# Performance work log

Measured on AMD Instinct MI355X. Metric: run time of the kernel, lower is better.

Reference implementation:

```python
import jax, jax.numpy as jnp
import numpy as np

N_HEAD = 16
D_HEAD = 64
D_MODEL = 1024
QLEN = 1024
BSZ = 4
RLEN = 1024
CONV = 7
SCALE = 1.0 / D_HEAD ** 0.5
NEG = -1e30
EPS = 1e-5


def setup_inputs() -> dict:
    key = jax.random.key(0)
    ks = jax.random.split(key, 14)
    s = 0.02
    inp = {
        "w": jax.random.normal(ks[0], (QLEN, BSZ, D_MODEL), jnp.float32),
        "r": jax.random.normal(ks[1], (RLEN, D_MODEL), jnp.float32),
        "r_w_bias": jax.random.normal(ks[2], (N_HEAD, D_HEAD), jnp.float32) * s,
        "r_r_bias": jax.random.normal(ks[3], (N_HEAD, D_HEAD), jnp.float32) * s,
        "W_qkv": jax.random.normal(ks[4], (3 * N_HEAD * D_HEAD, D_MODEL), jnp.float32) * s,
        "W_r": jax.random.normal(ks[5], (N_HEAD * D_HEAD, D_MODEL), jnp.float32) * s,
        "W_o": jax.random.normal(ks[6], (D_MODEL, N_HEAD * D_HEAD), jnp.float32) * s,
        "conv_wq": jax.random.normal(ks[7], (D_HEAD, D_HEAD, CONV), jnp.float32) * s,
        "conv_bq": jax.random.normal(ks[8], (D_HEAD,), jnp.float32) * s,
        "conv_wk": jax.random.normal(ks[9], (D_HEAD, D_HEAD, CONV), jnp.float32) * s,
        "conv_bk": jax.random.normal(ks[10], (D_HEAD,), jnp.float32) * s,
        "conv_wv": jax.random.normal(ks[11], (D_HEAD, D_HEAD, CONV), jnp.float32) * s,
        "conv_bv": jax.random.normal(ks[12], (D_HEAD,), jnp.float32) * s,
        "ln_gamma": jnp.ones((D_MODEL,), jnp.float32),
        "ln_beta": jnp.zeros((D_MODEL,), jnp.float32),
        # causal mask, True = masked out (original dim==3 branch: [qlen, klen, 1])
        "attn_mask": jnp.triu(jnp.ones((QLEN, QLEN), bool), k=1)[:, :, None],
    }
    return inp


def _conv1d(x, wgt, b):
    # x: [N, C, L], wgt: [O, I, K] (torch Conv1d layout), same padding
    y = jax.lax.conv_general_dilated(x, wgt, (1,), [(CONV // 2, CONV // 2)],
                                     dimension_numbers=("NCH", "OIH", "NCH"))
    return y + b[None, :, None]


def _rel_shift(x):
    # x: [q, k, b, n] -> Transformer-XL relative shift
    q, k, b, n = x.shape
    xp = jnp.concatenate([jnp.zeros((q, 1, b, n), x.dtype), x], axis=1)
    return xp.reshape(k + 1, q, b, n)[1:].reshape(q, k, b, n)


def reference(w, r, r_w_bias, r_r_bias, W_qkv, W_r, W_o,
              conv_wq, conv_bq, conv_wk, conv_bk, conv_wv, conv_bv,
              ln_gamma, ln_beta, attn_mask):
    qlen, bsz, _ = w.shape
    klen = qlen  # mems=None

    heads = jnp.einsum('qbm,hm->qbh', w, W_qkv)  # [q, b, 3*n*d]
    hq, hk, hv = jnp.split(heads, 3, axis=-1)

    def to_conv(x, L):
        # [L, b, n*d] -> [n*b, d, L]
        return x.reshape(L, bsz, N_HEAD, D_HEAD).transpose(2, 1, 3, 0).reshape(N_HEAD * bsz, D_HEAD, L)

    def from_conv(x, L):
        # [n*b, d, L] -> [L, b, n, d]
        return x.reshape(N_HEAD, bsz, D_HEAD, L).transpose(3, 1, 0, 2)

    q_h = from_conv(_conv1d(to_conv(hq, qlen), conv_wq, conv_bq), qlen)
    k_h = from_conv(_conv1d(to_conv(hk, klen), conv_wk, conv_bk), klen)
    v_h = from_conv(_conv1d(to_conv(hv, klen), conv_wv, conv_bv), klen)

    r_head_k = (r @ W_r.T).reshape(-1, N_HEAD, D_HEAD)  # [rlen, n, d]

    AC = jnp.einsum('ibnd,jbnd->ijbn', q_h + r_w_bias, k_h)
    BD = _rel_shift(jnp.einsum('ibnd,jnd->ijbn', q_h + r_r_bias, r_head_k))
    score = (AC + BD) * SCALE
    score = jnp.where(attn_mask[:, :, :, None], NEG, score)

    prob = jax.nn.softmax(score, axis=1)
    vec = jnp.einsum('ijbn,jbnd->ibnd', prob, v_h).reshape(qlen, bsz, N_HEAD * D_HEAD)
    attn_out = vec @ W_o.T

    x = w + attn_out
    mu = jnp.mean(x, axis=-1, keepdims=True)
    var = jnp.mean(jnp.square(x - mu), axis=-1, keepdims=True)
    return (x - mu) / jnp.sqrt(var + EPS) * ln_gamma + ln_beta
```

## Files before the change

### kernel.cpp

```cpp
#include <hip/hip_runtime.h>
#include <math.h>

#define L 1024
#define SCALEF 0.125f
#define NEGF -1e30f

typedef unsigned short u16;
typedef __bf16 bf16x8 __attribute__((ext_vector_type(8)));
typedef float f32x4 __attribute__((ext_vector_type(4)));
typedef unsigned short u16x8 __attribute__((ext_vector_type(8)));
typedef unsigned short u16x4 __attribute__((ext_vector_type(4)));

#define MFMA(a, b, c) __builtin_amdgcn_mfma_f32_16x16x32_bf16(a, b, c, 0, 0, 0)

__device__ inline u16 f2b(float f) {
  union { float f; unsigned u; } v; v.f = f;
  unsigned r = v.u + 0x7fffu + ((v.u >> 16) & 1u);
  return (u16)(r >> 16);
}

__device__ __forceinline__ void ld16(u16* lds, const u16* g) {
  __builtin_amdgcn_global_load_lds((const __attribute__((address_space(1))) unsigned int*)g,
                                   (__attribute__((address_space(3))) unsigned int*)lds, 16, 0, 0);
}

__global__ __launch_bounds__(256) void prep(const float* __restrict__ w, const float* __restrict__ Wqkv,
                                            const float* __restrict__ r, const float* __restrict__ Wr,
                                            const float* __restrict__ Wo,
                                            const float* __restrict__ cwq, const float* __restrict__ cwk,
                                            const float* __restrict__ cwv,
                                            u16* w_bf, u16* wqkv_bf, u16* r_bf, u16* wr_bf, u16* wo_bf,
                                            u16* wTq, u16* wTk, u16* wTv) {
  int i = blockIdx.x * 256 + threadIdx.x;
  if (i < 2621440) {
    const float* s; u16* d; int off;
    if (i < 1048576)      { s = w;    d = w_bf;    off = i; }
    else if (i < 1835008) { s = Wqkv; d = wqkv_bf; off = i - 1048576; }
    else if (i < 2097152) { s = r;    d = r_bf;    off = i - 1835008; }
    else if (i < 2359296) { s = Wr;   d = wr_bf;   off = i - 2097152; }
    else                  { s = Wo;   d = wo_bf;   off = i - 2359296; }
    float4 v = ((const float4*)s)[off];
    u16x4 o = {f2b(v.x), f2b(v.y), f2b(v.z), f2b(v.w)};
    ((u16x4*)d)[off] = o;
  } else {
    int j = i - 2621440;
    if (j < 86016) {
      int z = j / 28672, rem = j % 28672;
      const float* src = z == 0 ? cwq : z == 1 ? cwk : cwv;
      u16* dst = z == 0 ? wTq : z == 1 ? wTk : wTv;
      int tt = rem >> 12, rem2 = rem & 4095;
      int dout = rem2 >> 6, din = rem2 & 63;
      dst[rem] = f2b(src[(dout * 64 + din) * 7 + tt]);
    }
  }
}

template <int OB>
__device__ __forceinline__ void gemm256_tile(u16* lds, const u16* __restrict__ A,
                                             const u16* __restrict__ B, void* Cp,
                                             int N, int m0, int n0) {
  int t = threadIdx.x;
  int wv = t >> 6, lane = t & 63;
  int q4 = lane >> 4, li = lane & 15;
  int wm = wv >> 2, wn = wv & 3;
  int pc = (q4 ^ ((li >> 1) & 3)) << 3;
  int cs = (((t & 3) ^ ((t >> 3) & 3)) << 3);
  const u16* Ab = A + (size_t)(m0 + (t >> 2)) * 1024 + cs;
  const u16* Bb = B + (size_t)(n0 + (t >> 2)) * 1024 + cs;
  int wo = wv * 512;
  f32x4 acc[8][4];
#pragma unroll
  for (int m = 0; m < 8; ++m)
#pragma unroll
    for (int n = 0; n < 4; ++n) acc[m][n] = (f32x4){0.f, 0.f, 0.f, 0.f};
#define STAGE_A(kt) { int sl = ((kt) & 3) * 16384, kb = (kt) * 32; \
    ld16(lds + sl + wo, Ab + kb); ld16(lds + sl + 4096 + wo, Ab + 131072 + kb); }
#define STAGE_B(kt) { int sl = ((kt) & 3) * 16384 + 8192, kb = (kt) * 32; \
    ld16(lds + sl + wo, Bb + kb); ld16(lds + sl + 4096 + wo, Bb + 131072 + kb); }
  STAGE_A(0); STAGE_B(0); STAGE_A(1); STAGE_B(1);
  asm volatile("s_waitcnt vmcnt(4)" ::: "memory");
  __builtin_amdgcn_s_barrier();
  for (int kt = 0; kt < 32; ++kt) {
    const u16* sA = lds + (kt & 3) * 16384;
    const u16* sB = sA + 8192;
    bf16x8 fa[4], fb[4];
#pragma unroll
    for (int m = 0; m < 4; ++m) fa[m] = *(const bf16x8*)&sA[(wm * 128 + m * 16 + li) * 32 + pc];
#pragma unroll
    for (int n = 0; n < 4; ++n) fb[n] = *(const bf16x8*)&sB[(wn * 64 + n * 16 + li) * 32 + pc];
    if (kt < 30) STAGE_A(kt + 2);
    __builtin_amdgcn_s_barrier();
    __builtin_amdgcn_s_setprio(1);
#pragma unroll
    for (int m = 0; m < 4; ++m)
#pragma unroll
      for (int n = 0; n < 4; ++n) acc[m][n] = MFMA(fa[m], fb[n], acc[m][n]);
    __builtin_amdgcn_s_setprio(0);
    __builtin_amdgcn_s_barrier();
    bf16x8 fa2[4];
#pragma unroll
    for (int m = 0; m < 4; ++m) fa2[m] = *(const bf16x8*)&sA[(wm * 128 + 64 + m * 16 + li) * 32 + pc];
    if (kt < 30) {
      STAGE_B(kt + 2);
      asm volatile("s_waitcnt vmcnt(4)" ::: "memory");
    } else {
      asm volatile("s_waitcnt vmcnt(0)" ::: "memory");
    }
    __builtin_amdgcn_s_barrier();
    __builtin_amdgcn_s_setprio(1);
#pragma unroll
    for (int m = 0; m < 4; ++m)
#pragma unroll
      for (int n = 0; n < 4; ++n) acc[4 + m][n] = MFMA(fa2[m], fb[n], acc[4 + m][n]);
    __builtin_amdgcn_s_setprio(0);
    __builtin_amdgcn_s_barrier();
  }
#undef STAGE_A
#undef STAGE_B
#pragma unroll
  for (int m = 0; m < 8; ++m)
#pragma unroll
    for (int r = 0; r < 4; ++r) {
      size_t row = m0 + wm * 128 + m * 16 + q4 * 4 + r;
      if (OB) {
        u16* C = (u16*)Cp;
#pragma unroll
        for (int n = 0; n < 4; ++n) C[row * N + n0 + wn * 64 + n * 16 + li] = f2b(acc[m][n][r]);
      } else {
        float* C = (float*)Cp;
#pragma unroll
        for (int n = 0; n < 4; ++n) C[row * N + n0 + wn * 64 + n * 16 + li] = acc[m][n][r];
      }
    }
}

__global__ __launch_bounds__(512, 1) void gemm_stage1(const u16* __restrict__ w_bf,
                                                      const u16* __restrict__ wqkv_bf,
                                                      u16* __restrict__ heads,
                                                      const u16* __restrict__ r_bf,
                                                      const u16* __restrict__ wr_bf,
                                                      u16* __restrict__ rhk) {
  __shared__ u16 lds[65536];
  int id = blockIdx.x;
  if (id < 192) {
    gemm256_tile<1>(lds, w_bf, wqkv_bf, heads, 3072, (id / 12) << 8, (id % 12) << 8);
  } else {
    int j = id - 192;
    gemm256_tile<1>(lds, r_bf, wr_bf, rhk, 1024, (j >> 2) << 8, (j & 3) << 8);
  }
}

__global__ __launch_bounds__(256) void gemm_wo(const u16* __restrict__ A, const u16* __restrict__ B,
                                               float* __restrict__ C) {
  __shared__ u16 sA[2 * 64 * 32];
  __shared__ u16 sB[2 * 128 * 32];
  int t = threadIdx.x;
  int w = t >> 6, lane = t & 63;
  int q4 = lane >> 4, li = lane & 15;
  int m0 = blockIdx.y << 6, n0 = blockIdx.x << 7;
  int nw = w << 5;
  const int N = 1024, K = 1024;
  f32x4 acc[4][2];
#pragma unroll
  for (int i = 0; i < 4; ++i)
#pragma unroll
    for (int j = 0; j < 2; ++j) acc[i][j] = (f32x4){0.f, 0.f, 0.f, 0.f};
  int r0 = t >> 2, c0 = (t & 3) << 3;
  const u16* Ap = A + (size_t)(m0 + r0) * K + c0;
  const u16* Bp0 = B + (size_t)(n0 + r0) * K + c0;
  const u16* Bp1 = B + (size_t)(n0 + 64 + r0) * K + c0;
  int wo512 = w * 512;
  ld16(sA + wo512, Ap);
  ld16(sB + wo512, Bp0);
  ld16(sB + wo512 + 2048, Bp1);
  int cur = 0;
  for (int kb = 0; kb < K; kb += 32) {
    __syncthreads();
    int nxt = cur ^ 1;
    if (kb + 32 < K) {
      u16* nA = sA + nxt * 2048;
      u16* nB = sB + nxt * 4096;
      ld16(nA + wo512, Ap + kb + 32);
      ld16(nB + wo512, Bp0 + kb + 32);
      ld16(nB + wo512 + 2048, Bp1 + kb + 32);
    }
    const u16* cA = sA + cur * 2048;
    const u16* cB = sB + cur * 4096;
    bf16x8 fa[4], fb[2];
#pragma unroll
    for (int i = 0; i < 4; ++i) fa[i] = *(const bf16x8*)&cA[(i * 16 + li) * 32 + q4 * 8];
#pragma unroll
    for (int j = 0; j < 2; ++j) fb[j] = *(const bf16x8*)&cB[(nw + j * 16 + li) * 32 + q4 * 8];
#pragma unroll
    for (int mt = 0; mt < 4; ++mt)
#pragma unroll
      for (int nt = 0; nt < 2; ++nt) acc[mt][nt] = MFMA(fa[mt], fb[nt], acc[mt][nt]);
    cur = nxt;
  }
#pragma unroll
  for (int mt = 0; mt < 4; ++mt)
#pragma unroll
    for (int r = 0; r < 4; ++r) {
      size_t row = m0 + mt * 16 + q4 * 4 + r;
#pragma unroll
      for (int nt = 0; nt < 2; ++nt) C[row * N + n0 + nw + nt * 16 + li] = acc[mt][nt][r];
    }
}

__global__ __launch_bounds__(256) void conv3(const u16* __restrict__ x,
                                             const u16* __restrict__ wTq, const u16* __restrict__ wTk,
                                             const u16* __restrict__ wTv,
                                             const float* __restrict__ cbq, const float* __restrict__ cbk,
                                             const float* __restrict__ cbv,
                                             u16* __restrict__ qh, u16* __restrict__ kh, u16* __restrict__ vtg) {
  __shared__ u16 sX[70 * 72];
  int z = blockIdx.z;
  const u16* wT = z == 0 ? wTq : z == 1 ? wTk : wTv;
  const float* bias = z == 0 ? cbq : z == 1 ? cbk : cbv;
  int t = threadIdx.x;
  int w = t >> 6, lane = t & 63;
  int q4 = lane >> 4, li = lane & 15;
  int l0 = blockIdx.x << 6, bn = blockIdx.y;
  int b = bn >> 4, n = bn & 15;
  const u16* xb = x + b * 3072 + z * 1024 + n * 64;
  for (int e = t; e < 560; e += 256) {
    int ro = e >> 3, c = e & 7;
    int l = l0 - 3 + ro;
    u16x8 v = {0, 0, 0, 0, 0, 0, 0, 0};
    if (l >= 0 && l < L) v = *(const u16x8*)(xb + (size_t)l * 12288 + c * 8);
    *(u16x8*)&sX[ro * 72 + c * 8] = v;
  }
  bf16x8 Bw[7][2];
#pragma unroll
  for (int tt = 0; tt < 7; ++tt)
#pragma unroll
    for (int kc = 0; kc < 2; ++kc)
      Bw[tt][kc] = *(const bf16x8*)(wT + (tt * 64 + w * 16 + li) * 64 + kc * 32 + q4 * 8);
  f32x4 acc[4];
#pragma unroll
  for (int i = 0; i < 4; ++i) acc[i] = (f32x4){0.f, 0.f, 0.f, 0.f};
  __syncthreads();
#pragma unroll
  for (int tt = 0; tt < 7; ++tt)
#pragma unroll
    for (int kc = 0; kc < 2; ++kc)
#pragma unroll
      for (int mt = 0; mt < 4; ++mt) {
        bf16x8 a = *(const bf16x8*)&sX[(mt * 16 + li + tt) * 72 + kc * 32 + q4 * 8];
        acc[mt] = MFMA(a, Bw[tt][kc], acc[mt]);
      }
  float bv = bias[w * 16 + li];
  if (z < 2) {
    u16* out = z == 0 ? qh : kh;
#pragma unroll
    for (int mt = 0; mt < 4; ++mt)
#pragma unroll
      for (int r = 0; r < 4; ++r) {
        int l = l0 + mt * 16 + q4 * 4 + r;
        out[(((size_t)l * 4 + b) * 16 + n) * 64 + w * 16 + li] = f2b(acc[mt][r] + bv);
      }
  } else {
    __syncthreads();
#pragma unroll
    for (int mt = 0; mt < 4; ++mt)
#pragma unroll
      for (int r = 0; r < 4; ++r)
        sX[(w * 16 + li) * 72 + mt * 16 + q4 * 4 + r] = f2b(acc[mt][r] + bv);
    __syncthreads();
    int d = t >> 2, ch = t & 3;
    u16x8 v0 = *(u16x8*)&sX[d * 72 + ch * 16];
    u16x8 v1 = *(u16x8*)&sX[d * 72 + ch * 16 + 8];
    u16* dst = vtg + ((size_t)bn * 64 + d) * 1024 + l0 + ch * 16;
    *(u16x8*)dst = v0;
    *(u16x8*)(dst + 8) = v1;
  }
}

__global__ __launch_bounds__(256) void rel_attn(const u16* __restrict__ qh, const u16* __restrict__ kh,
                                                const u16* __restrict__ vt, const u16* __restrict__ rhk,
                                                const float* __restrict__ rwb_, const float* __restrict__ rrb_,
                                                u16* __restrict__ vec) {
  __shared__ u16 sK[64][72];
  __shared__ u16 sVt[64][72];
  __shared__ u16 sR[128][72];
  __shared__ u16 sP[4][16][72];
  int t = threadIdx.x;
  int w = t >> 6, lane = t & 63;
  int q4 = lane >> 4, li = lane & 15;
  int p = blockIdx.x, bn = blockIdx.y;
  int b = bn >> 4, n = bn & 15;
  int base_w = 48 - w * 16;
  const u16* vtb = vt + (size_t)bn * 64 * 1024;
  int er0 = t >> 3, ec = (t & 7) * 8;
  bf16x8 vone;
#pragma unroll
  for (int j = 0; j < 8; ++j) vone[j] = (__bf16)1.0f;
  float rwbv[2][8], rrbv[2][8];
#pragma unroll
  for (int kc = 0; kc < 2; ++kc)
#pragma unroll
    for (int j = 0; j < 8; ++j) {
      int d = kc * 32 + q4 * 8 + j;
      rwbv[kc][j] = rwb_[n * 64 + d];
      rrbv[kc][j] = rrb_[n * 64 + d];
    }
  for (int half = 0; half < 2; ++half) {
    int qt = (half == 0) ? p : 15 - p;
    int i0 = qt << 6;
    bf16x8 Aw[2], Ar[2];
    {
      const u16* qrow = qh + (((size_t)(i0 + w * 16 + li) * 4 + b) * 16 + n) * 64;
#pragma unroll
      for (int kc = 0; kc < 2; ++kc) {
        bf16x8 qv = *(const bf16x8*)(qrow + kc * 32 + q4 * 8);
        bf16x8 aw, ar;
#pragma unroll
        for (int j = 0; j < 8; ++j) {
          float qf = (float)qv[j];
          aw[j] = (__bf16)(qf + rwbv[kc][j]);
          ar[j] = (__bf16)(qf + rrbv[kc][j]);
        }
        Aw[kc] = aw;
        Ar[kc] = ar;
      }
    }
    f32x4 accO[4];
#pragma unroll
    for (int i = 0; i < 4; ++i) accO[i] = (f32x4){0.f, 0.f, 0.f, 0.f};
    f32x4 accL = (f32x4){0.f, 0.f, 0.f, 0.f};
    int ntile = qt + 1;
    u16x8 pK[2], pV[2], pR[4];
    {
      int j0 = 0, gB = 960 - i0;
#pragma unroll
      for (int i = 0; i < 2; ++i) {
        int row = er0 + i * 32;
        pK[i] = *(const u16x8*)(kh + (((size_t)(j0 + row) * 4 + b) * 16 + n) * 64 + ec);
        pV[i] = *(const u16x8*)(vtb + (size_t)row * 1024 + j0 + ec);
      }
#pragma unroll
      for (int i = 0; i < 4; ++i) {
        int m = er0 + i * 32;
        int g = gB + m;
        if (g > L - 1) g = L - 1;
        pR[i] = *(const u16x8*)(rhk + (size_t)g * 1024 + n * 64 + ec);
      }
    }
    for (int jt = 0; jt < ntile; ++jt) {
      __syncthreads();
#pragma unroll
      for (int i = 0; i < 2; ++i) {
        *(u16x8*)&sK[er0 + i * 32][ec] = pK[i];
        *(u16x8*)&sVt[er0 + i * 32][ec] = pV[i];
      }
#pragma unroll
      for (int i = 0; i < 4; ++i) *(u16x8*)&sR[er0 + i * 32][ec] = pR[i];
      __syncthreads();
      if (jt + 1 < ntile) {
        int j0 = (jt + 1) << 6, gB = 960 - i0 + j0;
#pragma unroll
        for (int i = 0; i < 2; ++i) {
          int row = er0 + i * 32;
          pK[i] = *(const u16x8*)(kh + (((size_t)(j0 + row) * 4 + b) * 16 + n) * 64 + ec);
          pV[i] = *(const u16x8*)(vtb + (size_t)row * 1024 + j0 + ec);
        }
#pragma unroll
        for (int i = 0; i < 4; ++i) {
          int m = er0 + i * 32;
          int g = gB + m;
          if (g > L - 1) g = L - 1;
          pR[i] = *(const u16x8*)(rhk + (size_t)g * 1024 + n * 64 + ec);
        }
      }
      int j0 = jt << 6;
      f32x4 accS[4], accG[5];
#pragma unroll
      for (int i = 0; i < 4; ++i) accS[i] = (f32x4){0.f, 0.f, 0.f, 0.f};
#pragma unroll
      for (int i = 0; i < 5; ++i) accG[i] = (f32x4){0.f, 0.f, 0.f, 0.f};
      __builtin_amdgcn_s_setprio(1);
#pragma unroll
      for (int kc = 0; kc < 2; ++kc) {
#pragma unroll
        for (int nt = 0; nt < 4; ++nt) {
          bf16x8 fk = *(const bf16x8*)&sK[nt * 16 + li][kc * 32 + q4 * 8];
          accS[nt] = MFMA(Aw[kc], fk, accS[nt]);
        }
#pragma unroll
        for (int nt = 0; nt < 5; ++nt) {
          bf16x8 fr = *(const bf16x8*)&sR[base_w + nt * 16 + li][kc * 32 + q4 * 8];
          accG[nt] = MFMA(Ar[kc], fr, accG[nt]);
        }
      }
      __builtin_amdgcn_s_setprio(0);
      float Sv[4][4];
#pragma unroll
      for (int nt = 0; nt < 4; ++nt)
#pragma unroll
        for (int r = 0; r < 4; ++r) {
          int il = q4 * 4 + r;
          int srcc = li + 15 - il;
          int lsrc = (lane & 48) | (srcc & 15);
          float pm = (li >= 15 - il) ? accG[nt][r] : accG[nt + 1][r];
          float g = __shfl(pm, lsrc);
          Sv[nt][r] = (accS[nt][r] + g) * SCALEF;
        }
      if (jt == qt) {
#pragma unroll
        for (int nt = 0; nt < 4; ++nt)
#pragma unroll
          for (int r = 0; r < 4; ++r)
            if (j0 + nt * 16 + li > i0 + w * 16 + q4 * 4 + r) Sv[nt][r] = NEGF;
      }
#pragma unroll
      for (int nt = 0; nt < 4; ++nt)
#pragma unroll
        for (int r = 0; r < 4; ++r) {
          float pv = __expf(Sv[nt][r]);
          sP[w][q4 * 4 + r][(nt * 16 + li) ^ (q4 << 3)] = f2b(pv);
        }
      __builtin_amdgcn_s_setprio(1);
#pragma unroll
      for (int kc = 0; kc < 2; ++kc) {
        bf16x8 ap = *(const bf16x8*)&sP[w][li][kc * 32 + ((q4 ^ ((li >> 2) & 3)) << 3)];
        accL = MFMA(ap, vone, accL);
#pragma unroll
        for (int nt = 0; nt < 4; ++nt) {
          bf16x8 fv = *(const bf16x8*)&sVt[nt * 16 + li][kc * 32 + q4 * 8];
          accO[nt] = MFMA(ap, fv, accO[nt]);
        }
      }
      __builtin_amdgcn_s_setprio(0);
    }
#pragma unroll
    for (int r = 0; r < 4; ++r) {
      int il = q4 * 4 + r;
      int ig = i0 + w * 16 + il;
      float inv = 1.0f / accL[r];
      u16* orow = vec + (((size_t)ig * 4 + b) * 16 + n) * 64;
#pragma unroll
      for (int nt = 0; nt < 4; ++nt) orow[nt * 16 + li] = f2b(accO[nt][r] * inv);
    }
  }
}

__global__ __launch_bounds__(256) void resid_ln(const float* __restrict__ w,
                                                const float* __restrict__ attn,
                                                const float* __restrict__ gamma,
                                                const float* __restrict__ beta,
                                                float* __restrict__ out) {
  __shared__ float ssum[4], ssq[4];
  int row = blockIdx.x, t = threadIdx.x;
  float4 xw = *(const float4*)&w[(size_t)row * 1024 + t * 4];
  float4 xa = *(const float4*)&attn[(size_t)row * 1024 + t * 4];
  float4 x = make_float4(xw.x + xa.x, xw.y + xa.y, xw.z + xa.z, xw.w + xa.w);
  float s = x.x + x.y + x.z + x.w;
  float sq = x.x * x.x + x.y * x.y + x.z * x.z + x.w * x.w;
#pragma unroll
  for (int off = 32; off > 0; off >>= 1) {
    s += __shfl_down(s, off);
    sq += __shfl_down(sq, off);
  }
  int wid = t >> 6;
  if ((t & 63) == 0) { ssum[wid] = s; ssq[wid] = sq; }
  __syncthreads();
  s = ssum[0] + ssum[1] + ssum[2] + ssum[3];
  sq = ssq[0] + ssq[1] + ssq[2] + ssq[3];
  float mean = s * (1.0f / 1024.0f);
  float var = sq * (1.0f / 1024.0f) - mean * mean;
  float rstd = rsqrtf(var + 1e-5f);
  float4 g = *(const float4*)&gamma[t * 4];
  float4 bb = *(const float4*)&beta[t * 4];
  float4 o;
  o.x = (x.x - mean) * rstd * g.x + bb.x;
  o.y = (x.y - mean) * rstd * g.y + bb.y;
  o.z = (x.z - mean) * rstd * g.z + bb.z;
  o.w = (x.w - mean) * rstd * g.w + bb.w;
  *(float4*)&out[(size_t)row * 1024 + t * 4] = o;
}

extern "C" void kernel_launch(void* const* d_in, const int* in_sizes, int n_in,
                              void* d_out, int out_size, void* d_ws, size_t ws_size,
                              hipStream_t stream) {
  const float* w     = (const float*)d_in[0];
  const float* r     = (const float*)d_in[1];
  const float* rwb   = (const float*)d_in[2];
  const float* rrb   = (const float*)d_in[3];
  const float* W_qkv = (const float*)d_in[4];
  const float* W_r   = (const float*)d_in[5];
  const float* W_o   = (const float*)d_in[6];
  const float* cwq   = (const float*)d_in[7];
  const float* cbq   = (const float*)d_in[8];
  const float* cwk   = (const float*)d_in[9];
  const float* cbk   = (const float*)d_in[10];
  const float* cwv   = (const float*)d_in[11];
  const float* cbv   = (const float*)d_in[12];
  const float* gamma = (const float*)d_in[13];
  const float* beta  = (const float*)d_in[14];
  float* outp = (float*)d_out;

  char* wsb = (char*)d_ws;
  u16*   heads   = (u16*)(wsb);
  u16*   vec     = (u16*)(wsb);
  float* attnf   = (float*)(wsb + 8388608);
  u16*   qh      = (u16*)(wsb + 25165824);
  u16*   kh      = (u16*)(wsb + 33554432);
  u16*   rhk     = (u16*)(wsb + 50331648);
  u16*   w_bf    = (u16*)(wsb + 52428800);
  u16*   wqkv_bf = (u16*)(wsb + 60817408);
  u16*   r_bf    = (u16*)(wsb + 67108864);
  u16*   wr_bf   = (u16*)(wsb + 69206016);
  u16*   wo_bf   = (u16*)(wsb + 71303168);
  u16*   wTq     = (u16*)(wsb + 73400320);
  u16*   wTk     = (u16*)(wsb + 73457664);
  u16*   wTv     = (u16*)(wsb + 73515008);
  u16*   vt      = (u16*)(wsb + 73572352);

  dim3 blk(256);
  prep<<<10576, blk, 0, stream>>>(w, W_qkv, r, W_r, W_o, cwq, cwk, cwv,
                                  w_bf, wqkv_bf, r_bf, wr_bf, wo_bf, wTq, wTk, wTv);
  gemm_stage1<<<208, dim3(512), 0, stream>>>(w_bf, wqkv_bf, heads, r_bf, wr_bf, rhk);
  conv3<<<dim3(16, 64, 3), blk, 0, stream>>>(heads, wTq, wTk, wTv, cbq, cbk, cbv, qh, kh, vt);
  rel_attn<<<dim3(8, 64), blk, 0, stream>>>(qh, kh, vt, rhk, rwb, rrb, vec);
  gemm_wo<<<dim3(8, 64), blk, 0, stream>>>(vec, wo_bf, attnf);
  resid_ln<<<4096, blk, 0, stream>>>(w, attnf, gamma, beta, outp);
}
```

Baseline: 249.9 us.

## Double-buffer K/R tiles in LDS and load V fragments directly from global

Double-buffers the K and R tiles in LDS and prefetches two tiles ahead, so each iteration needs one barrier instead of two. The V tile no longer goes through LDS: each wave loads its MFMA B-operand fragments for V straight from global memory into registers at the start of the iteration. This is meant to cut synchronization and LDS traffic. The cost is more register pressure and uncoalesced, redundant global loads of V across the four waves.

```diff
diff --git a/kernel.cpp b/kernel.cpp
--- a/kernel.cpp
+++ b/kernel.cpp
@@ -280,9 +280,8 @@
                                                 const u16* __restrict__ vt, const u16* __restrict__ rhk,
                                                 const float* __restrict__ rwb_, const float* __restrict__ rrb_,
                                                 u16* __restrict__ vec) {
-  __shared__ u16 sK[64][72];
-  __shared__ u16 sVt[64][72];
-  __shared__ u16 sR[128][72];
+  __shared__ u16 sK[2][64][72];
+  __shared__ u16 sR[2][128][72];
   __shared__ u16 sP[4][16][72];
   int t = threadIdx.x;
   int w = t >> 6, lane = t & 63;
@@ -304,6 +303,27 @@
       rwbv[kc][j] = rwb_[n * 64 + d];
       rrbv[kc][j] = rrb_[n * 64 + d];
     }
+  u16x8 pK[2], pR[4];
+#define LOADKR(JT) {                                                              \
+    int j0_ = (JT) << 6, gB_ = 960 - i0 + j0_;                                    \
+    _Pragma("unroll")                                                             \
+    for (int i_ = 0; i_ < 2; ++i_) {                                              \
+      int row_ = er0 + i_ * 32;                                                   \
+      pK[i_] = *(const u16x8*)(kh + (((size_t)(j0_ + row_) * 4 + b) * 16 + n) * 64 + ec); \
+    }                                                                             \
+    _Pragma("unroll")                                                             \
+    for (int i_ = 0; i_ < 4; ++i_) {                                              \
+      int g_ = gB_ + er0 + i_ * 32;                                               \
+      if (g_ > L - 1) g_ = L - 1;                                                 \
+      pR[i_] = *(const u16x8*)(rhk + (size_t)g_ * 1024 + n * 64 + ec);            \
+    }                                                                             \
+  }
+#define WRITEKR(BUF) {                                                            \
+    _Pragma("unroll")                                                             \
+    for (int i_ = 0; i_ < 2; ++i_) *(u16x8*)&sK[BUF][er0 + i_ * 32][ec] = pK[i_]; \
+    _Pragma("unroll")                                                             \
+    for (int i_ = 0; i_ < 4; ++i_) *(u16x8*)&sR[BUF][er0 + i_ * 32][ec] = pR[i_]; \
+  }
   for (int half = 0; half < 2; ++half) {
     int qt = (half == 0) ? p : 15 - p;
     int i0 = qt << 6;
@@ -329,50 +349,21 @@
     for (int i = 0; i < 4; ++i) accO[i] = (f32x4){0.f, 0.f, 0.f, 0.f};
     f32x4 accL = (f32x4){0.f, 0.f, 0.f, 0.f};
     int ntile = qt + 1;
-    u16x8 pK[2], pV[2], pR[4];
-    {
-      int j0 = 0, gB = 960 - i0;
-#pragma unroll
-      for (int i = 0; i < 2; ++i) {
-        int row = er0 + i * 32;
-        pK[i] = *(const u16x8*)(kh + (((size_t)(j0 + row) * 4 + b) * 16 + n) * 64 + ec);
-        pV[i] = *(const u16x8*)(vtb + (size_t)row * 1024 + j0 + ec);
-      }
-#pragma unroll
-      for (int i = 0; i < 4; ++i) {
-        int m = er0 + i * 32;
-        int g = gB + m;
-        if (g > L - 1) g = L - 1;
-        pR[i] = *(const u16x8*)(rhk + (size_t)g * 1024 + n * 64 + ec);
-      }
-    }
+    LOADKR(0);
+    WRITEKR(0);
+    if (ntile > 1) LOADKR(1);
+    __syncthreads();
     for (int jt = 0; jt < ntile; ++jt) {
-      __syncthreads();
-#pragma unroll
-      for (int i = 0; i < 2; ++i) {
-        *(u16x8*)&sK[er0 + i * 32][ec] = pK[i];
-        *(u16x8*)&sVt[er0 + i * 32][ec] = pV[i];
-      }
-#pragma unroll
-      for (int i = 0; i < 4; ++i) *(u16x8*)&sR[er0 + i * 32][ec] = pR[i];
-      __syncthreads();
-      if (jt + 1 < ntile) {
-        int j0 = (jt + 1) << 6, gB = 960 - i0 + j0;
-#pragma unroll
-        for (int i = 0; i < 2; ++i) {
-          int row = er0 + i * 32;
-          pK[i] = *(const u16x8*)(kh + (((size_t)(j0 + row) * 4 + b) * 16 + n) * 64 + ec);
-          pV[i] = *(const u16x8*)(vtb + (size_t)row * 1024 + j0 + ec);
-        }
-#pragma unroll
-        for (int i = 0; i < 4; ++i) {
-          int m = er0 + i * 32;
-          int g = gB + m;
-          if (g > L - 1) g = L - 1;
-          pR[i] = *(const u16x8*)(rhk + (size_t)g * 1024 + n * 64 + ec);
-        }
-      }
+      int cur = jt & 1;
       int j0 = jt << 6;
+      bf16x8 fvr[2][4];
+#pragma unroll
+      for (int kc = 0; kc < 2; ++kc)
+#pragma unroll
+        for (int nt = 0; nt < 4; ++nt)
+          fvr[kc][nt] = *(const bf16x8*)(vtb + (size_t)(nt * 16 + li) * 1024 + j0 + kc * 32 + q4 * 8);
+      if (jt + 1 < ntile) WRITEKR(cur ^ 1);
+      if (jt + 2 < ntile) LOADKR(jt + 2);
       f32x4 accS[4], accG[5];
 #pragma unroll
       for (int i = 0; i < 4; ++i) accS[i] = (f32x4){0.f, 0.f, 0.f, 0.f};
@@ -383,12 +374,12 @@
       for (int kc = 0; kc < 2; ++kc) {
 #pragma unroll
         for (int nt = 0; nt < 4; ++nt) {
-          bf16x8 fk = *(const bf16x8*)&sK[nt * 16 + li][kc * 32 + q4 * 8];
+          bf16x8 fk = *(const bf16x8*)&sK[cur][nt * 16 + li][kc * 32 + q4 * 8];
           accS[nt] = MFMA(Aw[kc], fk, accS[nt]);
         }
 #pragma unroll
         for (int nt = 0; nt < 5; ++nt) {
-          bf16x8 fr = *(const bf16x8*)&sR[base_w + nt * 16 + li][kc * 32 + q4 * 8];
+          bf16x8 fr = *(const bf16x8*)&sR[cur][base_w + nt * 16 + li][kc * 32 + q4 * 8];
           accG[nt] = MFMA(Ar[kc], fr, accG[nt]);
         }
       }
@@ -426,11 +417,11 @@
         accL = MFMA(ap, vone, accL);
 #pragma unroll
         for (int nt = 0; nt < 4; ++nt) {
-          bf16x8 fv = *(const bf16x8*)&sVt[nt * 16 + li][kc * 32 + q4 * 8];
-          accO[nt] = MFMA(ap, fv, accO[nt]);
+          accO[nt] = MFMA(ap, fvr[kc][nt], accO[nt]);
         }
       }
       __builtin_amdgcn_s_setprio(0);
+      __syncthreads();
     }
 #pragma unroll
     for (int r = 0; r < 4; ++r) {
@@ -442,6 +433,8 @@
       for (int nt = 0; nt < 4; ++nt) orow[nt * 16 + li] = f2b(accO[nt][r] * inv);
     }
   }
+#undef LOADKR
+#undef WRITEKR
 }
 
 __global__ __launch_bounds__(256) void resid_ln(const float* __restrict__ w,
```

Measured after the change: 275.2 us. 1.1x slower.

## Load V fragments directly from global, drop sVt LDS tile, raise occupancy

Applied to the files above, without the earlier changes.

Removes the shared-memory V^T tile and its register prefetch; each wave now loads its V MFMA fragments straight from global memory at the start of each key tile. Bias vectors are reloaded per half instead of kept in registers, and launch bounds request 4 blocks per SM. The goal is to cut LDS footprint and register pressure so more blocks fit per CU. The cost is redundant global/L2 reads of V across the four waves and less latency hiding for those loads.

```diff
diff --git a/kernel.cpp b/kernel.cpp
--- a/kernel.cpp
+++ b/kernel.cpp
@@ -276,12 +276,11 @@
   }
 }
 
-__global__ __launch_bounds__(256) void rel_attn(const u16* __restrict__ qh, const u16* __restrict__ kh,
-                                                const u16* __restrict__ vt, const u16* __restrict__ rhk,
-                                                const float* __restrict__ rwb_, const float* __restrict__ rrb_,
-                                                u16* __restrict__ vec) {
+__global__ __launch_bounds__(256, 4) void rel_attn(const u16* __restrict__ qh, const u16* __restrict__ kh,
+                                                   const u16* __restrict__ vt, const u16* __restrict__ rhk,
+                                                   const float* __restrict__ rwb_, const float* __restrict__ rrb_,
+                                                   u16* __restrict__ vec) {
   __shared__ u16 sK[64][72];
-  __shared__ u16 sVt[64][72];
   __shared__ u16 sR[128][72];
   __shared__ u16 sP[4][16][72];
   int t = threadIdx.x;
@@ -295,15 +294,6 @@
   bf16x8 vone;
 #pragma unroll
   for (int j = 0; j < 8; ++j) vone[j] = (__bf16)1.0f;
-  float rwbv[2][8], rrbv[2][8];
-#pragma unroll
-  for (int kc = 0; kc < 2; ++kc)
-#pragma unroll
-    for (int j = 0; j < 8; ++j) {
-      int d = kc * 32 + q4 * 8 + j;
-      rwbv[kc][j] = rwb_[n * 64 + d];
-      rrbv[kc][j] = rrb_[n * 64 + d];
-    }
   for (int half = 0; half < 2; ++half) {
     int qt = (half == 0) ? p : 15 - p;
     int i0 = qt << 6;
@@ -312,13 +302,19 @@
       const u16* qrow = qh + (((size_t)(i0 + w * 16 + li) * 4 + b) * 16 + n) * 64;
 #pragma unroll
       for (int kc = 0; kc < 2; ++kc) {
+        float4 w0 = *(const float4*)&rwb_[n * 64 + kc * 32 + q4 * 8];
+        float4 w1 = *(const float4*)&rwb_[n * 64 + kc * 32 + q4 * 8 + 4];
+        float4 r0 = *(const float4*)&rrb_[n * 64 + kc * 32 + q4 * 8];
+        float4 r1 = *(const float4*)&rrb_[n * 64 + kc * 32 + q4 * 8 + 4];
+        float rw[8] = {w0.x, w0.y, w0.z, w0.w, w1.x, w1.y, w1.z, w1.w};
+        float rr[8] = {r0.x, r0.y, r0.z, r0.w, r1.x, r1.y, r1.z, r1.w};
         bf16x8 qv = *(const bf16x8*)(qrow + kc * 32 + q4 * 8);
         bf16x8 aw, ar;
 #pragma unroll
         for (int j = 0; j < 8; ++j) {
           float qf = (float)qv[j];
-          aw[j] = (__bf16)(qf + rwbv[kc][j]);
-          ar[j] = (__bf16)(qf + rrbv[kc][j]);
+          aw[j] = (__bf16)(qf + rw[j]);
+          ar[j] = (__bf16)(qf + rr[j]);
         }
         Aw[kc] = aw;
         Ar[kc] = ar;
@@ -329,14 +325,13 @@
     for (int i = 0; i < 4; ++i) accO[i] = (f32x4){0.f, 0.f, 0.f, 0.f};
     f32x4 accL = (f32x4){0.f, 0.f, 0.f, 0.f};
     int ntile = qt + 1;
-    u16x8 pK[2], pV[2], pR[4];
+    u16x8 pK[2], pR[4];
     {
       int j0 = 0, gB = 960 - i0;
 #pragma unroll
       for (int i = 0; i < 2; ++i) {
         int row = er0 + i * 32;
         pK[i] = *(const u16x8*)(kh + (((size_t)(j0 + row) * 4 + b) * 16 + n) * 64 + ec);
-        pV[i] = *(const u16x8*)(vtb + (size_t)row * 1024 + j0 + ec);
       }
 #pragma unroll
       for (int i = 0; i < 4; ++i) {
@@ -349,20 +344,23 @@
     for (int jt = 0; jt < ntile; ++jt) {
       __syncthreads();
 #pragma unroll
-      for (int i = 0; i < 2; ++i) {
-        *(u16x8*)&sK[er0 + i * 32][ec] = pK[i];
-        *(u16x8*)&sVt[er0 + i * 32][ec] = pV[i];
-      }
+      for (int i = 0; i < 2; ++i) *(u16x8*)&sK[er0 + i * 32][ec] = pK[i];
 #pragma unroll
       for (int i = 0; i < 4; ++i) *(u16x8*)&sR[er0 + i * 32][ec] = pR[i];
       __syncthreads();
+      int j0 = jt << 6;
+      bf16x8 fvr[2][4];
+#pragma unroll
+      for (int kc = 0; kc < 2; ++kc)
+#pragma unroll
+        for (int nt = 0; nt < 4; ++nt)
+          fvr[kc][nt] = *(const bf16x8*)(vtb + (size_t)(nt * 16 + li) * 1024 + j0 + kc * 32 + q4 * 8);
       if (jt + 1 < ntile) {
-        int j0 = (jt + 1) << 6, gB = 960 - i0 + j0;
+        int j0n = (jt + 1) << 6, gB = 960 - i0 + j0n;
 #pragma unroll
         for (int i = 0; i < 2; ++i) {
           int row = er0 + i * 32;
-          pK[i] = *(const u16x8*)(kh + (((size_t)(j0 + row) * 4 + b) * 16 + n) * 64 + ec);
-          pV[i] = *(const u16x8*)(vtb + (size_t)row * 1024 + j0 + ec);
+          pK[i] = *(const u16x8*)(kh + (((size_t)(j0n + row) * 4 + b) * 16 + n) * 64 + ec);
         }
 #pragma unroll
         for (int i = 0; i < 4; ++i) {
@@ -372,7 +370,6 @@
           pR[i] = *(const u16x8*)(rhk + (size_t)g * 1024 + n * 64 + ec);
         }
       }
-      int j0 = jt << 6;
       f32x4 accS[4], accG[5];
 #pragma unroll
       for (int i = 0; i < 4; ++i) accS[i] = (f32x4){0.f, 0.f, 0.f, 0.f};
@@ -426,8 +423,7 @@
         accL = MFMA(ap, vone, accL);
 #pragma unroll
         for (int nt = 0; nt < 4; ++nt) {
-          bf16x8 fv = *(const bf16x8*)&sVt[nt * 16 + li][kc * 32 + q4 * 8];
-          accO[nt] = MFMA(ap, fv, accO[nt]);
+          accO[nt] = MFMA(ap, fvr[kc][nt], accO[nt]);
         }
       }
       __builtin_amdgcn_s_setprio(0);
```

After: 408.8 us. 1.64x slower.
